# Kernel optimization log

Measured on AMD Instinct MI355X. Metric: run time of the kernel, lower is better.

## Reference

```python
import jax, jax.numpy as jnp
import numpy as np

N = 65536      # nodes
E = 524288     # edges (avg degree 8)
C = 128        # in_channels == hidden_channels
L = 3          # num_layers
EPS = 1e-5     # BatchNorm eps


def setup_inputs() -> dict:
    key = jax.random.key(0)
    ks = jax.random.split(key, 12)
    inv = 1.0 / np.sqrt(C)
    return {
        "x": jax.random.normal(ks[0], (N, C), jnp.float32),
        "edge_weight": jax.random.uniform(ks[1], (E,), jnp.float32),
        "bn_gamma": 1.0 + 0.1 * jax.random.normal(ks[2], (L, C), jnp.float32),
        "bn_beta": 0.1 * jax.random.normal(ks[3], (L, C), jnp.float32),
        "W_self": inv * jax.random.normal(ks[4], (L, C, C), jnp.float32),
        "W_neigh": inv * jax.random.normal(ks[5], (L, C, C), jnp.float32),
        "bias": 0.01 * jax.random.normal(ks[6], (L, C), jnp.float32),
        "lin_w": inv * jax.random.normal(ks[7], (C,), jnp.float32),
        "lin_b": 0.01 * jax.random.normal(ks[8], (), jnp.float32),
        "src": jax.random.randint(ks[9], (E,), 0, N),
        "dst": jax.random.randint(ks[10], (E,), 0, N),
    }


def reference(x, edge_weight, bn_gamma, bn_beta, W_self, W_neigh, bias, lin_w, lin_b, src, dst):
    # log1p on edge weights (done once in the torch module per layer; identical each layer)
    ew = jnp.log1p(edge_weight)[:, None]                     # [E,1]
    # in-degree for mean aggregation (DGL fn.mean); isolated nodes -> divide by 1 (sum is 0)
    deg = jax.ops.segment_sum(jnp.ones((E,), x.dtype), dst, num_segments=N)
    deg = jnp.maximum(deg, 1.0)[:, None]                     # [N,1]

    h = x
    for l in range(L):
        # BatchNorm1d over nodes (training-mode batch stats, biased variance)
        mu = jnp.mean(h, axis=0)
        var = jnp.mean((h - mu) ** 2, axis=0)
        h = (h - mu) * jax.lax.rsqrt(var + EPS) * bn_gamma[l] + bn_beta[l]
        # SAGEConv mean aggregator: msg = h[src] * w, neigh = mean over in-edges
        msg = h[src] * ew                                    # [E,C]
        neigh = jax.ops.segment_sum(msg, dst, num_segments=N) / deg  # [N,C]
        h = jax.nn.relu(h @ W_self[l] + neigh @ W_neigh[l] + bias[l])
    return h @ lin_w + lin_b                                 # [N]
```

## Files before the change

kernel.cpp:

```cpp
#include <hip/hip_runtime.h>
#include <hip/hip_fp16.h>

#define NN 65536
#define EE 524288
#define CC 128
#define CAP 32
#define RPB 64
#define NBUCK 8

typedef _Float16 f16x8 __attribute__((ext_vector_type(8)));
typedef float f32x4 __attribute__((ext_vector_type(4)));


__global__ void k_init(const float* __restrict__ x, __half* __restrict__ h,
                       float* __restrict__ pstat0,
                       const int* __restrict__ src, const int* __restrict__ dst,
                       const float* __restrict__ ew,
                       int* __restrict__ cnt, unsigned int* __restrict__ buf) {
    int b = blockIdx.x, t = threadIdx.x;
    if (b < 256) {
        const float4* xv = (const float4*)x;
        __half2* o = (__half2*)h;
        float s[4] = {0, 0, 0, 0}, q[4] = {0, 0, 0, 0};
        for (int k = 0; k < 32; k++) {
            int i = b * 8192 + k * 256 + t;
            float4 v = xv[i];
            o[2 * i]     = __floats2half2_rn(v.x, v.y);
            o[2 * i + 1] = __floats2half2_rn(v.z, v.w);
            s[0] += v.x; s[1] += v.y; s[2] += v.z; s[3] += v.w;
            q[0] += v.x * v.x; q[1] += v.y * v.y; q[2] += v.z * v.z; q[3] += v.w * v.w;
        }
        __shared__ float ls[256];
        ls[t] = 0.f;
        __syncthreads();
        int c0 = (t & 31) * 4;
#pragma unroll
        for (int u = 0; u < 4; u++) {
            atomicAdd(&ls[c0 + u], s[u]);
            atomicAdd(&ls[128 + c0 + u], q[u]);
        }
        __syncthreads();
        if (t < 128) {
            atomicAdd(&pstat0[t], ls[t]);
            atomicAdd(&pstat0[128 + t], ls[128 + t]);
        }
    } else {
        int base = (b - 256) * 1024 + t;
        int dd[4], sr[4];
        float we[4];
#pragma unroll
        for (int u = 0; u < 4; u++) dd[u] = dst[base + u * 256];
#pragma unroll
        for (int u = 0; u < 4; u++) sr[u] = src[base + u * 256];
#pragma unroll
        for (int u = 0; u < 4; u++) we[u] = ew[base + u * 256];
        int pos[4];
#pragma unroll
        for (int u = 0; u < 4; u++) pos[u] = atomicAdd(&cnt[dd[u]], 1);
#pragma unroll
        for (int u = 0; u < 4; u++) {
            float w = log1pf(we[u]);
            unsigned int pk = (unsigned int)sr[u] |
                              ((unsigned int)__half_as_ushort(__float2half(w)) << 16);
            if (pos[u] < CAP) buf[dd[u] * CAP + pos[u]] = pk;
        }
    }
}


__global__ void k_fold(const float* __restrict__ pstat_l,
                       const float* __restrict__ gamma, const float* __restrict__ beta,
                       const float* __restrict__ Ws, const float* __restrict__ Wn,
                       const float* __restrict__ bias,
                       __half* __restrict__ Wcat, float* __restrict__ crow,
                       float* __restrict__ cneigh) {
    int bid = blockIdx.x;
    int tid = threadIdx.x;
    int c = bid * 2 + (tid >> 7);
    int k = tid & 127;
    float su = 0.f, sq = 0.f;
#pragma unroll
    for (int b = 0; b < NBUCK; b++) {
        su += pstat_l[b * 256 + k];
        sq += pstat_l[b * 256 + 128 + k];
    }
    float mu = su * (1.0f / NN);
    float var = sq * (1.0f / NN) - mu * mu;
    float alpha = rsqrtf(var + 1e-5f) * gamma[k];
    float delta = beta[k] - mu * alpha;
    float ws = Ws[k * 128 + c];
    float wn = Wn[k * 128 + c];
    Wcat[c * 256 + k]       = __float2half(alpha * ws);
    Wcat[c * 256 + 128 + k] = __float2half(alpha * wn);
    float rs = delta * ws, rn = delta * wn;
#pragma unroll
    for (int off = 1; off < 64; off <<= 1) {
        rs += __shfl_xor(rs, off);
        rn += __shfl_xor(rn, off);
    }
    __shared__ float tmp[8];
    int wv = tid >> 6;
    if ((tid & 63) == 0) { tmp[wv * 2] = rs; tmp[wv * 2 + 1] = rn; }
    __syncthreads();
    if ((tid & 127) == 0) {
        int base = (tid >> 7) * 4;
        crow[c]   = bias[c] + tmp[base + 0] + tmp[base + 2];
        cneigh[c] = tmp[base + 1] + tmp[base + 3];
    }
}

__launch_bounds__(256, 4)
__global__ void k_layer(const __half* __restrict__ hin,
                        const int* __restrict__ cnt,
                        const unsigned int* __restrict__ buf,
                        const __half* __restrict__ Wcat,
                        const float* __restrict__ crow, const float* __restrict__ cneigh,
                        float* __restrict__ sod, int writeSod,
                        const float* __restrict__ lin_w, const float* __restrict__ lin_b,
                        __half* __restrict__ hout, float* __restrict__ outv, int mode,
                        float* __restrict__ pstatN) {
    __shared__ __half aggT[RPB * 136];
    __shared__ float sodT[RPB];
    int tid = threadIdx.x;
    int lane = tid & 63;
    int wvid = tid >> 6;
    int l15 = lane & 15, quad = lane >> 4;
    int i0 = blockIdx.x * RPB;
    int rbase = i0 + wvid * 16;

    f16x8 as0[4];
#pragma unroll
    for (int s = 0; s < 4; s++) {
        int kof = s * 32 + quad * 8;
        as0[s] = *(const f16x8*)&hin[(rbase + l15) * 128 + kof];
    }

    const __half2* h2 = (const __half2*)hin;
    int dv = 0;
    if (lane < 16) { dv = cnt[rbase + lane]; if (dv > CAP) dv = CAP; }
    int dA = __shfl(dv, 0), dB = __shfl(dv, 1);
    unsigned int pkA = 0, pkB = 0;
    if (lane < dA) pkA = buf[(rbase + 0) * CAP + lane];
    if (lane < dB) pkB = buf[(rbase + 1) * CAP + lane];

    for (int pair = 0; pair < 8; ++pair) {
        int ndA = 0, ndB = 0;
        unsigned int npA = 0, npB = 0;
        if (pair < 7) {
            ndA = __shfl(dv, 2 * pair + 2);
            ndB = __shfl(dv, 2 * pair + 3);
            if (lane < ndA) npA = buf[(rbase + 2 * pair + 2) * CAP + lane];
            if (lane < ndB) npB = buf[(rbase + 2 * pair + 3) * CAP + lane];
        }
        float ax[8], ay[8], bx[8], by[8];
#pragma unroll
        for (int u = 0; u < 8; u++) { ax[u] = 0.f; ay[u] = 0.f; bx[u] = 0.f; by[u] = 0.f; }
        int dmax = dA > dB ? dA : dB;
        int rounds = (dmax + 7) >> 3;
        for (int r = 0; r < rounds; r++) {
            int j = r * 8;
            unsigned int pA[8], pB[8];
            __half2 hA[8], hB[8];
#pragma unroll
            for (int u = 0; u < 8; u++) pA[u] = __shfl(pkA, j + u);
#pragma unroll
            for (int u = 0; u < 8; u++) pB[u] = __shfl(pkB, j + u);
#pragma unroll
            for (int u = 0; u < 8; u++) hA[u] = h2[(pA[u] & 0xFFFF) * 64 + lane];
#pragma unroll
            for (int u = 0; u < 8; u++) hB[u] = h2[(pB[u] & 0xFFFF) * 64 + lane];
#pragma unroll
            for (int u = 0; u < 8; u++) {
                float w = __half2float(__ushort_as_half((unsigned short)(pA[u] >> 16)));
                float2 v = __half22float2(hA[u]);
                ax[u] += w * v.x;
                ay[u] += w * v.y;
            }
#pragma unroll
            for (int u = 0; u < 8; u++) {
                float w = __half2float(__ushort_as_half((unsigned short)(pB[u] >> 16)));
                float2 v = __half22float2(hB[u]);
                bx[u] += w * v.x;
                by[u] += w * v.y;
            }
        }
        float axs = ((ax[0] + ax[1]) + (ax[2] + ax[3])) + ((ax[4] + ax[5]) + (ax[6] + ax[7]));
        float ays = ((ay[0] + ay[1]) + (ay[2] + ay[3])) + ((ay[4] + ay[5]) + (ay[6] + ay[7]));
        float bxs = ((bx[0] + bx[1]) + (bx[2] + bx[3])) + ((bx[4] + bx[5]) + (bx[6] + bx[7]));
        float bys = ((by[0] + by[1]) + (by[2] + by[3])) + ((by[4] + by[5]) + (by[6] + by[7]));
        float invA = 1.0f / (float)(dA > 1 ? dA : 1);
        float invB = 1.0f / (float)(dB > 1 ? dB : 1);
        int rloc = wvid * 16 + 2 * pair;
        *(__half2*)&aggT[rloc * 136 + 2 * lane]       = __floats2half2_rn(axs * invA, ays * invA);
        *(__half2*)&aggT[(rloc + 1) * 136 + 2 * lane] = __floats2half2_rn(bxs * invB, bys * invB);
        if (writeSod) {
            float wA = __half2float(__ushort_as_half((unsigned short)(pkA >> 16)));
            float wB = __half2float(__ushort_as_half((unsigned short)(pkB >> 16)));
#pragma unroll
            for (int off = 1; off < 64; off <<= 1) {
                wA += __shfl_xor(wA, off);
                wB += __shfl_xor(wB, off);
            }
            if (lane == 0) {
                sodT[rloc] = wA * invA;     sod[i0 + rloc] = wA * invA;
                sodT[rloc + 1] = wB * invB; sod[i0 + rloc + 1] = wB * invB;
            }
        }
        dA = ndA; dB = ndB; pkA = npA; pkB = npB;
    }

    f32x4 acc[8];
    f32x4 zero = {0.f, 0.f, 0.f, 0.f};
#pragma unroll
    for (int t = 0; t < 8; t++) acc[t] = zero;

#pragma unroll
    for (int s = 0; s < 4; s++) {
        int kof = s * 32 + quad * 8;
#pragma unroll
        for (int tn = 0; tn < 8; tn++) {
            f16x8 bf = *(const f16x8*)&Wcat[(tn * 16 + l15) * 256 + kof];
            acc[tn] = __builtin_amdgcn_mfma_f32_16x16x32_f16(as0[s], bf, acc[tn], 0, 0, 0);
        }
    }
#pragma unroll
    for (int s = 0; s < 4; s++) {
        int kof = s * 32 + quad * 8;
        f16x8 an0 = *(const f16x8*)&aggT[(wvid * 16 + l15) * 136 + kof];
#pragma unroll
        for (int tn = 0; tn < 8; tn++) {
            f16x8 bf = *(const f16x8*)&Wcat[(tn * 16 + l15) * 256 + 128 + kof];
            acc[tn] = __builtin_amdgcn_mfma_f32_16x16x32_f16(an0, bf, acc[tn], 0, 0, 0);
        }
    }

    float cr[8], cn[8];
#pragma unroll
    for (int tn = 0; tn < 8; tn++) {
        cr[tn] = crow[tn * 16 + l15];
        cn[tn] = cneigh[tn * 16 + l15];
    }
    int rwbase = i0 + wvid * 16 + quad * 4;

    if (mode == 0) {
        float cs[8], cq[8];
#pragma unroll
        for (int tn = 0; tn < 8; tn++) { cs[tn] = 0.f; cq[tn] = 0.f; }
#pragma unroll
        for (int r = 0; r < 4; r++) {
            int row = rwbase + r;
            float sdv = writeSod ? sodT[row - i0] : sod[row];
#pragma unroll
            for (int tn = 0; tn < 8; tn++) {
                float v = acc[tn][r] + cr[tn] + sdv * cn[tn];
                v = fmaxf(v, 0.f);
                hout[row * 128 + tn * 16 + l15] = __float2half(v);
                cs[tn] += v;
                cq[tn] += v * v;
            }
        }
#pragma unroll
        for (int tn = 0; tn < 8; tn++) {
            cs[tn] += __shfl_xor(cs[tn], 16); cs[tn] += __shfl_xor(cs[tn], 32);
            cq[tn] += __shfl_xor(cq[tn], 16); cq[tn] += __shfl_xor(cq[tn], 32);
        }
        float* st = (float*)aggT;
        __syncthreads();
        st[tid] = 0.f;
        __syncthreads();
        if (lane < 16) {
#pragma unroll
            for (int tn = 0; tn < 8; tn++) {
                atomicAdd(&st[tn * 16 + l15], cs[tn]);
                atomicAdd(&st[128 + tn * 16 + l15], cq[tn]);
            }
        }
        __syncthreads();
        if (tid < 128) {
            float* pb = pstatN + ((blockIdx.x & (NBUCK - 1)) << 8);
            atomicAdd(&pb[tid], st[tid]);
            atomicAdd(&pb[128 + tid], st[128 + tid]);
        }
    } else {
        float lw[8];
#pragma unroll
        for (int tn = 0; tn < 8; tn++) lw[tn] = lin_w[tn * 16 + l15];
        float lb = lin_b[0];
#pragma unroll
        for (int r = 0; r < 4; r++) {
            int row = rwbase + r;
            float sdv = sod[row];
            float p = 0.f;
#pragma unroll
            for (int tn = 0; tn < 8; tn++) {
                float v = acc[tn][r] + cr[tn] + sdv * cn[tn];
                v = fmaxf(v, 0.f);
                p += v * lw[tn];
            }
            p += __shfl_xor(p, 1);
            p += __shfl_xor(p, 2);
            p += __shfl_xor(p, 4);
            p += __shfl_xor(p, 8);
            if (l15 == 0) outv[row] = p + lb;
        }
    }
}


extern "C" void kernel_launch(void* const* d_in, const int* in_sizes, int n_in,
                              void* d_out, int out_size, void* d_ws, size_t ws_size,
                              hipStream_t stream) {
    (void)in_sizes; (void)n_in; (void)out_size; (void)ws_size;
    const float* x     = (const float*)d_in[0];
    const float* ew    = (const float*)d_in[1];
    const float* gamma = (const float*)d_in[2];
    const float* beta  = (const float*)d_in[3];
    const float* Ws    = (const float*)d_in[4];
    const float* Wn    = (const float*)d_in[5];
    const float* bias  = (const float*)d_in[6];
    const float* lin_w = (const float*)d_in[7];
    const float* lin_b = (const float*)d_in[8];
    const int*   srcI  = (const int*)d_in[9];
    const int*   dstI  = (const int*)d_in[10];
    float* out = (float*)d_out;

    char* p = (char*)d_ws;
    __half* ha   = (__half*)p; p += (size_t)NN * CC * 2;
    __half* hb   = (__half*)p; p += (size_t)NN * CC * 2;
    __half* Wcat = (__half*)p; p += 256 * 128 * 2;
    float* crow   = (float*)p; p += 512;
    float* cneigh = (float*)p; p += 512;
    float* sod    = (float*)p; p += (size_t)NN * 4;
    unsigned int* buf = (unsigned int*)p; p += (size_t)NN * CAP * 4;
    int*   cnt    = (int*)p;   p += (size_t)NN * 4;
    float* pstat  = (float*)p; p += 3 * NBUCK * 256 * 4;

    hipMemsetAsync(cnt, 0, (size_t)NN * 4 + 3 * NBUCK * 256 * 4, stream);

    k_init<<<dim3(256 + EE / 1024), dim3(256), 0, stream>>>(x, ha, pstat, srcI, dstI, ew, cnt, buf);

    const __half* hin = ha;
    __half* hout = hb;
    for (int l = 0; l < 3; l++) {
        k_fold<<<dim3(64), dim3(256), 0, stream>>>(
            pstat + (size_t)l * NBUCK * 256, gamma + l * CC, beta + l * CC,
            Ws + (size_t)l * CC * CC, Wn + (size_t)l * CC * CC, bias + l * CC,
            Wcat, crow, cneigh);
        int mode = (l == 2) ? 1 : 0;
        float* pstatN = (mode == 0) ? (pstat + (size_t)(l + 1) * NBUCK * 256) : pstat;
        k_layer<<<dim3(NN / RPB), dim3(256), 0, stream>>>(
            hin, cnt, buf, Wcat, crow, cneigh, sod, (l == 0) ? 1 : 0,
            lin_w, lin_b, hout, out, mode, pstatN);
        const __half* t = hin; hin = hout; hout = (__half*)t;
    }
}
```

Before: 293.0 us.

## Gather neighbors with 16-byte loads, four rows per wave concurrently

Restructures the neighbor aggregation so each wave handles four destination rows at a time, one per 16-lane quad. Each lane loads 8 fp16 channels as a 16-byte vector instead of one half2, which cuts the number of gather instructions and raises memory-level parallelism. The trip count of the edge loop is now the maximum degree across the four rows, so lanes whose row has fewer edges do masked work. The intent is higher gather throughput in this memory-bound step, at the cost of more registers per lane.

```diff
diff --git a/kernel.cpp b/kernel.cpp
--- a/kernel.cpp
+++ b/kernel.cpp
@@ -135,78 +135,61 @@
         as0[s] = *(const f16x8*)&hin[(rbase + l15) * 128 + kof];
     }
 
-    const __half2* h2 = (const __half2*)hin;
-    int dv = 0;
-    if (lane < 16) { dv = cnt[rbase + lane]; if (dv > CAP) dv = CAP; }
-    int dA = __shfl(dv, 0), dB = __shfl(dv, 1);
-    unsigned int pkA = 0, pkB = 0;
-    if (lane < dA) pkA = buf[(rbase + 0) * CAP + lane];
-    if (lane < dB) pkB = buf[(rbase + 1) * CAP + lane];
-
-    for (int pair = 0; pair < 8; ++pair) {
-        int ndA = 0, ndB = 0;
-        unsigned int npA = 0, npB = 0;
-        if (pair < 7) {
-            ndA = __shfl(dv, 2 * pair + 2);
-            ndB = __shfl(dv, 2 * pair + 3);
-            if (lane < ndA) npA = buf[(rbase + 2 * pair + 2) * CAP + lane];
-            if (lane < ndB) npB = buf[(rbase + 2 * pair + 3) * CAP + lane];
-        }
-        float ax[8], ay[8], bx[8], by[8];
-#pragma unroll
-        for (int u = 0; u < 8; u++) { ax[u] = 0.f; ay[u] = 0.f; bx[u] = 0.f; by[u] = 0.f; }
-        int dmax = dA > dB ? dA : dB;
-        int rounds = (dmax + 7) >> 3;
-        for (int r = 0; r < rounds; r++) {
-            int j = r * 8;
-            unsigned int pA[8], pB[8];
-            __half2 hA[8], hB[8];
-#pragma unroll
-            for (int u = 0; u < 8; u++) pA[u] = __shfl(pkA, j + u);
-#pragma unroll
-            for (int u = 0; u < 8; u++) pB[u] = __shfl(pkB, j + u);
-#pragma unroll
-            for (int u = 0; u < 8; u++) hA[u] = h2[(pA[u] & 0xFFFF) * 64 + lane];
-#pragma unroll
-            for (int u = 0; u < 8; u++) hB[u] = h2[(pB[u] & 0xFFFF) * 64 + lane];
-#pragma unroll
-            for (int u = 0; u < 8; u++) {
-                float w = __half2float(__ushort_as_half((unsigned short)(pA[u] >> 16)));
-                float2 v = __half22float2(hA[u]);
-                ax[u] += w * v.x;
-                ay[u] += w * v.y;
+    const f16x8* hv = (const f16x8*)hin;
+    int dv = cnt[rbase + l15]; if (dv > CAP) dv = CAP;
+    unsigned int pkg0, pkg1, pkg2, pkg3;
+    pkg0 = buf[(rbase + 0 * 4 + quad) * CAP + l15];
+    pkg1 = buf[(rbase + 1 * 4 + quad) * CAP + l15];
+    pkg2 = buf[(rbase + 2 * 4 + quad) * CAP + l15];
+    pkg3 = buf[(rbase + 3 * 4 + quad) * CAP + l15];
+
+#pragma unroll
+    for (int g = 0; g < 4; g++) {
+        unsigned int pk = (g == 0) ? pkg0 : (g == 1) ? pkg1 : (g == 2) ? pkg2 : pkg3;
+        int dq = __shfl(dv, g * 4 + quad);
+        int t0 = __shfl_xor(dq, 16); int dm = dq > t0 ? dq : t0;
+        int t1 = __shfl_xor(dm, 32); dm = dm > t1 ? dm : t1;
+        unsigned int pk2 = 0;
+        if (dm > 16) pk2 = buf[(rbase + g * 4 + quad) * CAP + 16 + l15];
+        float acc[8];
+#pragma unroll
+        for (int u = 0; u < 8; u++) acc[u] = 0.f;
+        int nch = (dm + 7) >> 3;
+        for (int c = 0; c < nch; ++c) {
+            unsigned int sreg = (c & 2) ? pk2 : pk;
+            int sbase = (quad << 4) + ((c & 1) << 3);
+            int e0 = c * 8;
+            unsigned int pe[8];
+#pragma unroll
+            for (int e = 0; e < 8; e++) pe[e] = __shfl(sreg, sbase + e);
+#pragma unroll
+            for (int e = 0; e < 8; e++) if (e0 + e >= dq) pe[e] = 0;
+            f16x8 ve[8];
+#pragma unroll
+            for (int e = 0; e < 8; e++) ve[e] = hv[(pe[e] & 0xFFFF) * 16 + l15];
+#pragma unroll
+            for (int e = 0; e < 8; e++) {
+                float w = (e0 + e < dq)
+                    ? __half2float(__ushort_as_half((unsigned short)(pe[e] >> 16))) : 0.f;
+#pragma unroll
+                for (int u = 0; u < 8; u++) acc[u] += w * (float)ve[e][u];
             }
-#pragma unroll
-            for (int u = 0; u < 8; u++) {
-                float w = __half2float(__ushort_as_half((unsigned short)(pB[u] >> 16)));
-                float2 v = __half22float2(hB[u]);
-                bx[u] += w * v.x;
-                by[u] += w * v.y;
-            }
-        }
-        float axs = ((ax[0] + ax[1]) + (ax[2] + ax[3])) + ((ax[4] + ax[5]) + (ax[6] + ax[7]));
-        float ays = ((ay[0] + ay[1]) + (ay[2] + ay[3])) + ((ay[4] + ay[5]) + (ay[6] + ay[7]));
-        float bxs = ((bx[0] + bx[1]) + (bx[2] + bx[3])) + ((bx[4] + bx[5]) + (bx[6] + bx[7]));
-        float bys = ((by[0] + by[1]) + (by[2] + by[3])) + ((by[4] + by[5]) + (by[6] + by[7]));
-        float invA = 1.0f / (float)(dA > 1 ? dA : 1);
-        float invB = 1.0f / (float)(dB > 1 ? dB : 1);
-        int rloc = wvid * 16 + 2 * pair;
-        *(__half2*)&aggT[rloc * 136 + 2 * lane]       = __floats2half2_rn(axs * invA, ays * invA);
-        *(__half2*)&aggT[(rloc + 1) * 136 + 2 * lane] = __floats2half2_rn(bxs * invB, bys * invB);
+        }
+        float inv = 1.0f / (float)(dq > 1 ? dq : 1);
+        int rloc = wvid * 16 + g * 4 + quad;
+        f16x8 o;
+#pragma unroll
+        for (int u = 0; u < 8; u++) o[u] = (_Float16)(acc[u] * inv);
+        *(f16x8*)&aggT[rloc * 136 + l15 * 8] = o;
         if (writeSod) {
-            float wA = __half2float(__ushort_as_half((unsigned short)(pkA >> 16)));
-            float wB = __half2float(__ushort_as_half((unsigned short)(pkB >> 16)));
-#pragma unroll
-            for (int off = 1; off < 64; off <<= 1) {
-                wA += __shfl_xor(wA, off);
-                wB += __shfl_xor(wB, off);
-            }
-            if (lane == 0) {
-                sodT[rloc] = wA * invA;     sod[i0 + rloc] = wA * invA;
-                sodT[rloc + 1] = wB * invB; sod[i0 + rloc + 1] = wB * invB;
-            }
-        }
-        dA = ndA; dB = ndB; pkA = npA; pkB = npB;
+            float ws = (l15 < dq)
+                ? __half2float(__ushort_as_half((unsigned short)(pk >> 16))) : 0.f;
+            if (16 + l15 < dq)
+                ws += __half2float(__ushort_as_half((unsigned short)(pk2 >> 16)));
+            ws += __shfl_xor(ws, 1); ws += __shfl_xor(ws, 2);
+            ws += __shfl_xor(ws, 4); ws += __shfl_xor(ws, 8);
+            if (l15 == 0) { sodT[rloc] = ws * inv; sod[i0 + rloc] = ws * inv; }
+        }
     }
 
     f32x4 acc[8];
```

Measured after the change: 290.7 us. No clear change (-0.8%).
